# Kernel tuning notes

Measured on AMD Instinct MI355X. Metric: run time of the kernel, lower is better.

Reference implementation:

```python
import jax, jax.numpy as jnp
import numpy as np

B, TD, SD, H = 512, 2048, 768, 128


def setup_inputs() -> dict:
    key = jax.random.key(0)
    ks = jax.random.split(key, 12)
    s = lambda k, shape, fan_in: jax.random.normal(k, shape, jnp.float32) * (1.0 / np.sqrt(fan_in))
    return {
        "teacher_features": jax.random.normal(ks[0], (B, TD), jnp.float32),
        "student_features": jax.random.normal(ks[1], (B, SD), jnp.float32),
        # Linear weights stored [in, out] (transposed vs torch) so y = x @ W + b
        "Wt": s(ks[2], (TD, H), TD), "bt": jnp.zeros((H,), jnp.float32),
        "Ws": s(ks[3], (SD, H), SD), "bs": jnp.zeros((H,), jnp.float32),
        "W1": s(ks[4], (2 * H, H), 2 * H), "b1": jnp.zeros((H,), jnp.float32),
        "W2": s(ks[5], (H, 1), H), "b2": jnp.zeros((1,), jnp.float32),
    }


def reference(teacher_features, student_features, Wt, bt, Ws, bs, W1, b1, W2, b2):
    def compute_relations(f):
        b, h = f.shape
        # pairwise concat [f_i, f_j] -> [B, B, 2H]
        pair = jnp.concatenate(
            [jnp.broadcast_to(f[:, None, :], (b, b, h)),
             jnp.broadcast_to(f[None, :, :], (b, b, h))], axis=-1)
        hdn = jax.nn.relu(jnp.einsum('ijk,kh->ijh', pair, W1) + b1)
        rel = jax.nn.sigmoid(jnp.einsum('ijh,ho->ijo', hdn, W2) + b2)[..., 0]
        # diagonal stays zero (i != j in the original loop)
        return rel * (1.0 - jnp.eye(b, dtype=rel.dtype))

    tp = teacher_features @ Wt + bt  # [B, H]
    sp = student_features @ Ws + bs  # [B, H]
    t_rel = compute_relations(tp)
    s_rel = compute_relations(sp)
    return jnp.mean((s_rel - t_rel) ** 2)
```

## Files before the change

### kernel.cpp

```cpp
#include <hip/hip_runtime.h>

#define HDIM 128
#define BDIM 512

typedef __attribute__((ext_vector_type(8))) __bf16 bf16x8;
typedef __attribute__((ext_vector_type(4))) float  f32x4;

template<int K>
__device__ __forceinline__ f32x4 proj_acc(const float* __restrict__ F,
                                          const float* __restrict__ W,
                                          int m0, int n0, int wv, int l)
{
    constexpr int Ks = K >> 2;
    const int q = l >> 4, ln = l & 15;
    const float* Fp = &F[(size_t)(m0 + ln) * K + wv * Ks + q * 8];
    const float* Wp = &W[(size_t)(wv * Ks + q * 8) * HDIM + n0 + ln];
    f32x4 acc = {0.f, 0.f, 0.f, 0.f};
    #pragma unroll
    for (int k0 = 0; k0 < Ks; k0 += 32) {
        const float4 fa0 = *(const float4*)(Fp + k0);
        const float4 fa1 = *(const float4*)(Fp + k0 + 4);
        bf16x8 a, b;
        a[0] = (__bf16)fa0.x; a[1] = (__bf16)fa0.y; a[2] = (__bf16)fa0.z; a[3] = (__bf16)fa0.w;
        a[4] = (__bf16)fa1.x; a[5] = (__bf16)fa1.y; a[6] = (__bf16)fa1.z; a[7] = (__bf16)fa1.w;
        #pragma unroll
        for (int j = 0; j < 8; ++j)
            b[j] = (__bf16)Wp[(size_t)(k0 + j) * HDIM];
        acc = __builtin_amdgcn_mfma_f32_16x16x32_bf16(a, b, acc, 0, 0, 0);
    }
    return acc;
}

__global__ __launch_bounds__(256) void proj_mfma(
    const float* __restrict__ Ft, const float* __restrict__ Fs,
    const float* __restrict__ Wt, const float* __restrict__ Ws,
    __bf16* __restrict__ Pbt, __bf16* __restrict__ Pbs)
{
    const int tid = threadIdx.x;
    const int wv = tid >> 6, l = tid & 63;

    const int bid = blockIdx.x;
    const int c  = bid & 7;
    const int tt = bid >> 3;
    const int ntile = tt & 7;
    const int g  = ((tt >> 3) << 3) + c;
    const int net = g >> 5, mtile = g & 31;

    const int m0 = mtile * 16, n0 = ntile * 16;

    f32x4 acc;
    __bf16* P;
    if (net == 0) { acc = proj_acc<2048>(Ft, Wt, m0, n0, wv, l); P = Pbt; }
    else          { acc = proj_acc<768 >(Fs, Ws, m0, n0, wv, l); P = Pbs; }

    __shared__ float lds[4 * 256];
    #pragma unroll
    for (int r = 0; r < 4; ++r) lds[wv * 256 + r * 64 + l] = acc[r];
    __syncthreads();

    {
        const float s = lds[tid] + lds[256 + tid] + lds[512 + tid] + lds[768 + tid];
        const int r = tid >> 6, l2 = tid & 63;
        const int row = m0 + ((l2 >> 4) << 2) + r;
        const int col = n0 + (l2 & 15);
        P[(size_t)row * HDIM + col] = (__bf16)s;
    }
}

__global__ __launch_bounds__(64) void uv_mfma(
    const __bf16* __restrict__ Pbt, const __bf16* __restrict__ Pbs,
    const float* __restrict__ bt, const float* __restrict__ bs,
    const float* __restrict__ W1, const float* __restrict__ b1,
    float* __restrict__ Ut, float* __restrict__ Vt,
    float* __restrict__ Us, float* __restrict__ Vs,
    float* __restrict__ out)
{
    const int t = blockIdx.x;
    const int net = t >> 9, uvh = (t >> 8) & 1;
    const int mtile = (t >> 3) & 31, ntile = t & 7;
    const int l = threadIdx.x;

    if (t == 0 && l == 0) out[0] = 0.f;

    const __bf16* P   = net ? Pbs : Pbt;
    const float* bias = net ? bs : bt;
    float* O = net ? (uvh ? Vs : Us) : (uvh ? Vt : Ut);
    const float* W1o = W1 + (size_t)uvh * HDIM * HDIM;

    const int m0 = mtile * 16, n0 = ntile * 16;
    const int q = l >> 4, ln = l & 15;
    const int arow = m0 + ln, bn = n0 + ln;

    f32x4 acc = {0.f, 0.f, 0.f, 0.f};
    float cpart = 0.f;
    #pragma unroll
    for (int k0 = 0; k0 < HDIM; k0 += 32) {
        const int ka = k0 + q * 8;
        bf16x8 a = *(const bf16x8*)&P[(size_t)arow * HDIM + ka];
        bf16x8 b;
        #pragma unroll
        for (int j = 0; j < 8; ++j) {
            const float w = W1o[(size_t)(ka + j) * HDIM + bn];
            b[j] = (__bf16)w;
            cpart = fmaf(bias[ka + j], w, cpart);
        }
        acc = __builtin_amdgcn_mfma_f32_16x16x32_bf16(a, b, acc, 0, 0, 0);
    }
    cpart += __shfl_xor(cpart, 16, 64);
    cpart += __shfl_xor(cpart, 32, 64);
    const float cfull = cpart + (uvh == 0 ? b1[bn] : 0.f);

    #pragma unroll
    for (int r = 0; r < 4; ++r) {
        const int row = m0 + q * 4 + r;
        O[(size_t)row * HDIM + bn] = acc[r] + cfull;
    }
}

__global__ __launch_bounds__(512) void pair_kernel(
    const float* __restrict__ Ut, const float* __restrict__ Vt,
    const float* __restrict__ Us, const float* __restrict__ Vs,
    const float* __restrict__ W2, const float* __restrict__ b2,
    float* __restrict__ out)
{
    __shared__ alignas(16) float4 tUt[32 * 17];
    __shared__ alignas(16) float4 tVt[32 * 17];
    __shared__ alignas(16) float4 tUs[32 * 17];
    __shared__ alignas(16) float4 tVs[32 * 17];
    __shared__ alignas(16) float4 w2s[32];
    __shared__ float red[512];

    const int tx = threadIdx.x, ty = threadIdx.y;
    const int tid = ty * 16 + tx;
    const int i0 = blockIdx.y * 32, j0 = blockIdx.x * 32;

    const float4* Ut4 = (const float4*)Ut;
    const float4* Vt4 = (const float4*)Vt;
    const float4* Us4 = (const float4*)Us;
    const float4* Vs4 = (const float4*)Vs;

    if (tid < 32) w2s[tid] = ((const float4*)W2)[tid];

    float aT[2] = {0.f, 0.f};
    float aS[2] = {0.f, 0.f};

    for (int half = 0; half < 2; ++half) {
        const int c0 = half * 16;
        __syncthreads();
        {
            const int r = tid >> 4, cc = tid & 15;
            tUt[r * 17 + cc] = Ut4[(size_t)(i0 + r) * 32 + c0 + cc];
            tVt[r * 17 + cc] = Vt4[(size_t)(j0 + r) * 32 + c0 + cc];
            tUs[r * 17 + cc] = Us4[(size_t)(i0 + r) * 32 + c0 + cc];
            tVs[r * 17 + cc] = Vs4[(size_t)(j0 + r) * 32 + c0 + cc];
        }
        __syncthreads();

        #pragma unroll 4
        for (int h4 = 0; h4 < 16; ++h4) {
            float4 w  = w2s[c0 + h4];
            float4 u  = tUt[ty * 17 + h4];
            float4 p  = tUs[ty * 17 + h4];
            float4 v0 = tVt[tx * 17 + h4];
            float4 v1 = tVt[(tx + 16) * 17 + h4];
            float4 q0 = tVs[tx * 17 + h4];
            float4 q1 = tVs[(tx + 16) * 17 + h4];

            aT[0] = fmaf(fmaxf(u.x + v0.x, 0.f), w.x,
                    fmaf(fmaxf(u.y + v0.y, 0.f), w.y,
                    fmaf(fmaxf(u.z + v0.z, 0.f), w.z,
                    fmaf(fmaxf(u.w + v0.w, 0.f), w.w, aT[0]))));
            aT[1] = fmaf(fmaxf(u.x + v1.x, 0.f), w.x,
                    fmaf(fmaxf(u.y + v1.y, 0.f), w.y,
                    fmaf(fmaxf(u.z + v1.z, 0.f), w.z,
                    fmaf(fmaxf(u.w + v1.w, 0.f), w.w, aT[1]))));
            aS[0] = fmaf(fmaxf(p.x + q0.x, 0.f), w.x,
                    fmaf(fmaxf(p.y + q0.y, 0.f), w.y,
                    fmaf(fmaxf(p.z + q0.z, 0.f), w.z,
                    fmaf(fmaxf(p.w + q0.w, 0.f), w.w, aS[0]))));
            aS[1] = fmaf(fmaxf(p.x + q1.x, 0.f), w.x,
                    fmaf(fmaxf(p.y + q1.y, 0.f), w.y,
                    fmaf(fmaxf(p.z + q1.z, 0.f), w.z,
                    fmaf(fmaxf(p.w + q1.w, 0.f), w.w, aS[1]))));
        }
    }

    const float b2v = b2[0];
    float local = 0.f;
    #pragma unroll
    for (int b = 0; b < 2; ++b) {
        const int i = i0 + ty;
        const int j = j0 + tx + 16 * b;
        if (i != j) {
            float tr = 1.f / (1.f + __expf(-(aT[b] + b2v)));
            float sr = 1.f / (1.f + __expf(-(aS[b] + b2v)));
            float d = sr - tr;
            local = fmaf(d, d, local);
        }
    }

    red[tid] = local;
    __syncthreads();
    #pragma unroll
    for (int s = 256; s > 0; s >>= 1) {
        if (tid < s) red[tid] += red[tid + s];
        __syncthreads();
    }
    if (tid == 0)
        atomicAdd(out, red[0] * (1.0f / ((float)BDIM * (float)BDIM)));
}

extern "C" void kernel_launch(void* const* d_in, const int* in_sizes, int n_in,
                              void* d_out, int out_size, void* d_ws, size_t ws_size,
                              hipStream_t stream) {
    const float* teacher = (const float*)d_in[0];
    const float* student = (const float*)d_in[1];
    const float* Wt = (const float*)d_in[2];
    const float* bt = (const float*)d_in[3];
    const float* Ws = (const float*)d_in[4];
    const float* bs = (const float*)d_in[5];
    const float* W1 = (const float*)d_in[6];
    const float* b1 = (const float*)d_in[7];
    const float* W2 = (const float*)d_in[8];
    const float* b2 = (const float*)d_in[9];
    float* out = (float*)d_out;

    const size_t M = (size_t)BDIM * HDIM;
    __bf16* Pbt = (__bf16*)d_ws;
    __bf16* Pbs = Pbt + M;
    float* Ut = (float*)(Pbs + M);
    float* Vt = Ut + M;
    float* Us = Vt + M;
    float* Vs = Us + M;

    proj_mfma<<<512, 256, 0, stream>>>(teacher, student, Wt, Ws, Pbt, Pbs);

    uv_mfma<<<1024, 64, 0, stream>>>(Pbt, Pbs, bt, bs, W1, b1,
                                     Ut, Vt, Us, Vs, out);

    pair_kernel<<<dim3(16, 16), dim3(16, 32), 0, stream>>>(
        Ut, Vt, Us, Vs, W2, b2, out);
}
```

Measured before the change: 97.11 us.

## Store U/V as bf16 and use packed 2-wide FP32 math in pair kernel

The intermediate U/V projections are now written as bf16 instead of fp32, which halves their storage and load traffic. The pair kernel now loads the full 128-wide rows into LDS in one pass and unpacks bf16 pairs into float2 values. It computes a 2x2 register tile per thread with packed float2 add/max/fma to use dual-issue FP32. Block size drops to 256 threads and W2 is read directly from global memory; the bf16 rounding of U/V adds numerical error.

```diff
diff --git a/kernel.cpp b/kernel.cpp
--- a/kernel.cpp
+++ b/kernel.cpp
@@ -5,6 +5,7 @@
 
 typedef __attribute__((ext_vector_type(8))) __bf16 bf16x8;
 typedef __attribute__((ext_vector_type(4))) float  f32x4;
+typedef __attribute__((ext_vector_type(2))) float  f32x2;
 
 template<int K>
 __device__ __forceinline__ f32x4 proj_acc(const float* __restrict__ F,
@@ -71,8 +72,8 @@
     const __bf16* __restrict__ Pbt, const __bf16* __restrict__ Pbs,
     const float* __restrict__ bt, const float* __restrict__ bs,
     const float* __restrict__ W1, const float* __restrict__ b1,
-    float* __restrict__ Ut, float* __restrict__ Vt,
-    float* __restrict__ Us, float* __restrict__ Vs,
+    __bf16* __restrict__ Ut, __bf16* __restrict__ Vt,
+    __bf16* __restrict__ Us, __bf16* __restrict__ Vs,
     float* __restrict__ out)
 {
     const int t = blockIdx.x;
@@ -84,7 +85,7 @@
 
     const __bf16* P   = net ? Pbs : Pbt;
     const float* bias = net ? bs : bt;
-    float* O = net ? (uvh ? Vs : Us) : (uvh ? Vt : Ut);
+    __bf16* O = net ? (uvh ? Vs : Us) : (uvh ? Vt : Ut);
     const float* W1o = W1 + (size_t)uvh * HDIM * HDIM;
 
     const int m0 = mtile * 16, n0 = ntile * 16;
@@ -113,96 +114,109 @@
     #pragma unroll
     for (int r = 0; r < 4; ++r) {
         const int row = m0 + q * 4 + r;
-        O[(size_t)row * HDIM + bn] = acc[r] + cfull;
-    }
-}
-
-__global__ __launch_bounds__(512) void pair_kernel(
-    const float* __restrict__ Ut, const float* __restrict__ Vt,
-    const float* __restrict__ Us, const float* __restrict__ Vs,
+        O[(size_t)row * HDIM + bn] = (__bf16)(acc[r] + cfull);
+    }
+}
+
+__device__ __forceinline__ f32x2 bfpair(unsigned d) {
+    f32x2 r;
+    r.x = __uint_as_float(d << 16);
+    r.y = __uint_as_float(d & 0xffff0000u);
+    return r;
+}
+
+__global__ __launch_bounds__(256) void pair_kernel(
+    const __bf16* __restrict__ Ut, const __bf16* __restrict__ Vt,
+    const __bf16* __restrict__ Us, const __bf16* __restrict__ Vs,
     const float* __restrict__ W2, const float* __restrict__ b2,
     float* __restrict__ out)
 {
-    __shared__ alignas(16) float4 tUt[32 * 17];
-    __shared__ alignas(16) float4 tVt[32 * 17];
-    __shared__ alignas(16) float4 tUs[32 * 17];
-    __shared__ alignas(16) float4 tVs[32 * 17];
-    __shared__ alignas(16) float4 w2s[32];
-    __shared__ float red[512];
+    __shared__ alignas(16) unsigned short tU[32 * 136];
+    __shared__ alignas(16) unsigned short tV[32 * 136];
+    __shared__ alignas(16) unsigned short tP[32 * 136];
+    __shared__ alignas(16) unsigned short tQ[32 * 136];
+    __shared__ float red[256];
 
     const int tx = threadIdx.x, ty = threadIdx.y;
     const int tid = ty * 16 + tx;
     const int i0 = blockIdx.y * 32, j0 = blockIdx.x * 32;
 
-    const float4* Ut4 = (const float4*)Ut;
-    const float4* Vt4 = (const float4*)Vt;
-    const float4* Us4 = (const float4*)Us;
-    const float4* Vs4 = (const float4*)Vs;
-
-    if (tid < 32) w2s[tid] = ((const float4*)W2)[tid];
-
-    float aT[2] = {0.f, 0.f};
-    float aS[2] = {0.f, 0.f};
-
-    for (int half = 0; half < 2; ++half) {
-        const int c0 = half * 16;
-        __syncthreads();
-        {
-            const int r = tid >> 4, cc = tid & 15;
-            tUt[r * 17 + cc] = Ut4[(size_t)(i0 + r) * 32 + c0 + cc];
-            tVt[r * 17 + cc] = Vt4[(size_t)(j0 + r) * 32 + c0 + cc];
-            tUs[r * 17 + cc] = Us4[(size_t)(i0 + r) * 32 + c0 + cc];
-            tVs[r * 17 + cc] = Vs4[(size_t)(j0 + r) * 32 + c0 + cc];
-        }
-        __syncthreads();
-
-        #pragma unroll 4
-        for (int h4 = 0; h4 < 16; ++h4) {
-            float4 w  = w2s[c0 + h4];
-            float4 u  = tUt[ty * 17 + h4];
-            float4 p  = tUs[ty * 17 + h4];
-            float4 v0 = tVt[tx * 17 + h4];
-            float4 v1 = tVt[(tx + 16) * 17 + h4];
-            float4 q0 = tVs[tx * 17 + h4];
-            float4 q1 = tVs[(tx + 16) * 17 + h4];
-
-            aT[0] = fmaf(fmaxf(u.x + v0.x, 0.f), w.x,
-                    fmaf(fmaxf(u.y + v0.y, 0.f), w.y,
-                    fmaf(fmaxf(u.z + v0.z, 0.f), w.z,
-                    fmaf(fmaxf(u.w + v0.w, 0.f), w.w, aT[0]))));
-            aT[1] = fmaf(fmaxf(u.x + v1.x, 0.f), w.x,
-                    fmaf(fmaxf(u.y + v1.y, 0.f), w.y,
-                    fmaf(fmaxf(u.z + v1.z, 0.f), w.z,
-                    fmaf(fmaxf(u.w + v1.w, 0.f), w.w, aT[1]))));
-            aS[0] = fmaf(fmaxf(p.x + q0.x, 0.f), w.x,
-                    fmaf(fmaxf(p.y + q0.y, 0.f), w.y,
-                    fmaf(fmaxf(p.z + q0.z, 0.f), w.z,
-                    fmaf(fmaxf(p.w + q0.w, 0.f), w.w, aS[0]))));
-            aS[1] = fmaf(fmaxf(p.x + q1.x, 0.f), w.x,
-                    fmaf(fmaxf(p.y + q1.y, 0.f), w.y,
-                    fmaf(fmaxf(p.z + q1.z, 0.f), w.z,
-                    fmaf(fmaxf(p.w + q1.w, 0.f), w.w, aS[1]))));
-        }
+    #pragma unroll
+    for (int it = 0; it < 2; ++it) {
+        const int s = tid + it * 256;
+        const int r = s >> 4, c8 = s & 15;
+        *(uint4*)&tU[r * 136 + c8 * 8] = *(const uint4*)&Ut[(size_t)(i0 + r) * HDIM + c8 * 8];
+        *(uint4*)&tV[r * 136 + c8 * 8] = *(const uint4*)&Vt[(size_t)(j0 + r) * HDIM + c8 * 8];
+        *(uint4*)&tP[r * 136 + c8 * 8] = *(const uint4*)&Us[(size_t)(i0 + r) * HDIM + c8 * 8];
+        *(uint4*)&tQ[r * 136 + c8 * 8] = *(const uint4*)&Vs[(size_t)(j0 + r) * HDIM + c8 * 8];
+    }
+    __syncthreads();
+
+    f32x2 aT[2][2] = {{{0.f,0.f},{0.f,0.f}},{{0.f,0.f},{0.f,0.f}}};
+    f32x2 aS[2][2] = {{{0.f,0.f},{0.f,0.f}},{{0.f,0.f},{0.f,0.f}}};
+    const f32x2 z2 = {0.f, 0.f};
+    const float4* W24 = (const float4*)W2;
+
+    #pragma unroll
+    for (int h8 = 0; h8 < 16; ++h8) {
+        const float4 wA = W24[h8 * 2 + 0];
+        const float4 wB = W24[h8 * 2 + 1];
+        const f32x2 w[4] = {{wA.x, wA.y}, {wA.z, wA.w}, {wB.x, wB.y}, {wB.z, wB.w}};
+
+        const uint4 du0 = *(const uint4*)&tU[(ty     ) * 136 + h8 * 8];
+        const uint4 du1 = *(const uint4*)&tU[(ty + 16) * 136 + h8 * 8];
+        const uint4 dv0 = *(const uint4*)&tV[(tx     ) * 136 + h8 * 8];
+        const uint4 dv1 = *(const uint4*)&tV[(tx + 16) * 136 + h8 * 8];
+        const uint4 dp0 = *(const uint4*)&tP[(ty     ) * 136 + h8 * 8];
+        const uint4 dp1 = *(const uint4*)&tP[(ty + 16) * 136 + h8 * 8];
+        const uint4 dq0 = *(const uint4*)&tQ[(tx     ) * 136 + h8 * 8];
+        const uint4 dq1 = *(const uint4*)&tQ[(tx + 16) * 136 + h8 * 8];
+
+        f32x2 u[2][4], v[2][4], p[2][4], q[2][4];
+        u[0][0] = bfpair(du0.x); u[0][1] = bfpair(du0.y); u[0][2] = bfpair(du0.z); u[0][3] = bfpair(du0.w);
+        u[1][0] = bfpair(du1.x); u[1][1] = bfpair(du1.y); u[1][2] = bfpair(du1.z); u[1][3] = bfpair(du1.w);
+        v[0][0] = bfpair(dv0.x); v[0][1] = bfpair(dv0.y); v[0][2] = bfpair(dv0.z); v[0][3] = bfpair(dv0.w);
+        v[1][0] = bfpair(dv1.x); v[1][1] = bfpair(dv1.y); v[1][2] = bfpair(dv1.z); v[1][3] = bfpair(dv1.w);
+        p[0][0] = bfpair(dp0.x); p[0][1] = bfpair(dp0.y); p[0][2] = bfpair(dp0.z); p[0][3] = bfpair(dp0.w);
+        p[1][0] = bfpair(dp1.x); p[1][1] = bfpair(dp1.y); p[1][2] = bfpair(dp1.z); p[1][3] = bfpair(dp1.w);
+        q[0][0] = bfpair(dq0.x); q[0][1] = bfpair(dq0.y); q[0][2] = bfpair(dq0.z); q[0][3] = bfpair(dq0.w);
+        q[1][0] = bfpair(dq1.x); q[1][1] = bfpair(dq1.y); q[1][2] = bfpair(dq1.z); q[1][3] = bfpair(dq1.w);
+
+        #pragma unroll
+        for (int a = 0; a < 2; ++a)
+            #pragma unroll
+            for (int b = 0; b < 2; ++b)
+                #pragma unroll
+                for (int k = 0; k < 4; ++k) {
+                    f32x2 m1 = __builtin_elementwise_max(u[a][k] + v[b][k], z2);
+                    aT[a][b] = __builtin_elementwise_fma(m1, w[k], aT[a][b]);
+                    f32x2 m2 = __builtin_elementwise_max(p[a][k] + q[b][k], z2);
+                    aS[a][b] = __builtin_elementwise_fma(m2, w[k], aS[a][b]);
+                }
     }
 
     const float b2v = b2[0];
     float local = 0.f;
     #pragma unroll
-    for (int b = 0; b < 2; ++b) {
-        const int i = i0 + ty;
-        const int j = j0 + tx + 16 * b;
-        if (i != j) {
-            float tr = 1.f / (1.f + __expf(-(aT[b] + b2v)));
-            float sr = 1.f / (1.f + __expf(-(aS[b] + b2v)));
-            float d = sr - tr;
-            local = fmaf(d, d, local);
+    for (int a = 0; a < 2; ++a)
+        #pragma unroll
+        for (int b = 0; b < 2; ++b) {
+            const int i = i0 + ty + 16 * a;
+            const int j = j0 + tx + 16 * b;
+            if (i != j) {
+                const float sT = aT[a][b].x + aT[a][b].y;
+                const float sS = aS[a][b].x + aS[a][b].y;
+                const float tr = 1.f / (1.f + __expf(-(sT + b2v)));
+                const float sr = 1.f / (1.f + __expf(-(sS + b2v)));
+                const float d = sr - tr;
+                local = fmaf(d, d, local);
+            }
         }
-    }
 
     red[tid] = local;
     __syncthreads();
     #pragma unroll
-    for (int s = 256; s > 0; s >>= 1) {
+    for (int s = 128; s > 0; s >>= 1) {
         if (tid < s) red[tid] += red[tid + s];
         __syncthreads();
     }
@@ -228,16 +242,16 @@
     const size_t M = (size_t)BDIM * HDIM;
     __bf16* Pbt = (__bf16*)d_ws;
     __bf16* Pbs = Pbt + M;
-    float* Ut = (float*)(Pbs + M);
-    float* Vt = Ut + M;
-    float* Us = Vt + M;
-    float* Vs = Us + M;
+    __bf16* Ut = Pbs + M;
+    __bf16* Vt = Ut + M;
+    __bf16* Us = Vt + M;
+    __bf16* Vs = Us + M;
 
     proj_mfma<<<512, 256, 0, stream>>>(teacher, student, Wt, Ws, Pbt, Pbs);
 
     uv_mfma<<<1024, 64, 0, stream>>>(Pbt, Pbs, bt, bs, W1, b1,
                                      Ut, Vt, Us, Vs, out);
 
-    pair_kernel<<<dim3(16, 16), dim3(16, 32), 0, stream>>>(
+    pair_kernel<<<dim3(16, 16), dim3(16, 16), 0, stream>>>(
         Ut, Vt, Us, Vs, W2, b2, out);
 }
```

Result: slower. 221.9 us (+128.5%).
